# Optimization experiments

Measured on AMD Instinct MI355X. Metric: run time of the kernel, lower is better.

Reference implementation:

```python
import jax, jax.numpy as jnp
import numpy as np

B_SZ, L, D_MODEL = 2, 2048, 2048
INTER, HEADS, P, N, G, K = 4096, 64, 64, 128, 1, 4
CONV_DIM = INTER + 2 * G * N
EPS = 1e-5


def silu(x):
    return x * jax.nn.sigmoid(x)


def softplus_thresh(x, threshold=10.0):
    # matches source: where(x < thr, log(1+exp(x)), x)
    return jnp.where(x < threshold, jnp.log1p(jnp.exp(jnp.minimum(x, threshold))), x)


def setup_inputs() -> dict:
    key = jax.random.key(0)
    ks = jax.random.split(key, 8)
    s = 0.02
    return {
        "hidden_states": jax.random.normal(ks[0], (B_SZ, L, D_MODEL), jnp.float32),
        "W_z": jax.random.normal(ks[1], (D_MODEL, INTER), jnp.float32) * s,
        "W_xBC": jax.random.normal(ks[2], (D_MODEL, CONV_DIM), jnp.float32) * s,
        "W_dt": jax.random.normal(ks[3], (D_MODEL, HEADS), jnp.float32) * s,
        "conv_w": jax.random.normal(ks[4], (CONV_DIM, K), jnp.float32) * 0.1,
        "conv_b": jnp.zeros((CONV_DIM,), jnp.float32),
        "dt_bias": jax.random.uniform(ks[5], (HEADS,), jnp.float32, -2.0, 0.0),
        "A_log": jnp.log(jnp.arange(1, HEADS + 1, dtype=jnp.float32)),
        "D": jnp.ones((HEADS,), jnp.float32),
        "norm_w": jnp.ones((INTER,), jnp.float32),
        "W_out": jax.random.normal(ks[6], (INTER, D_MODEL), jnp.float32) * s,
    }


def reference(hidden_states, W_z, W_xBC, W_dt, conv_w, conv_b, dt_bias, A_log, D, norm_w, W_out):
    b, l, _ = hidden_states.shape
    Hg = HEADS // G  # heads per group

    gate = hidden_states @ W_z                      # [b,l,INTER]
    xBC = hidden_states @ W_xBC                     # [b,l,CONV_DIM]
    dt = softplus_thresh(hidden_states @ W_dt + dt_bias)  # [b,l,H]

    # causal depthwise conv1d + silu (padding=K-1, truncated to seq_len)
    xp = jnp.pad(xBC, ((0, 0), (K - 1, 0), (0, 0)))
    kern = jnp.transpose(conv_w)[:, None, :]        # [K,1,CONV_DIM] (WIO)
    xBC = jax.lax.conv_general_dilated(
        xp, kern, (1,), 'VALID',
        dimension_numbers=('NWC', 'WIO', 'NWC'),
        feature_group_count=CONV_DIM)
    xBC = silu(xBC + conv_b)

    gns = G * N
    x = xBC[..., :INTER].reshape(b, l, G, Hg, P)
    Bm = xBC[..., INTER:INTER + gns].reshape(b, l, G, N)
    Cm = xBC[..., INTER + gns:].reshape(b, l, G, N)

    A = -jnp.exp(A_log)                             # [H]
    dA = jnp.exp(dt * A).reshape(b, l, G, Hg)       # [b,l,G,Hg]
    dtx = dt.reshape(b, l, G, Hg)[..., None] * x    # [b,l,G,Hg,P]

    def step(state, inp):
        dA_t, dtx_t, B_t, C_t = inp
        # state: [b,G,Hg,P,N]
        state = state * dA_t[..., None, None] + dtx_t[..., None] * B_t[:, :, None, None, :]
        y_t = jnp.einsum('bghpn,bgn->bghp', state, C_t)
        return state, y_t

    xs = (jnp.moveaxis(dA, 1, 0), jnp.moveaxis(dtx, 1, 0),
          jnp.moveaxis(Bm, 1, 0), jnp.moveaxis(Cm, 1, 0))
    state0 = jnp.zeros((b, G, Hg, P, N), jnp.float32)
    _, ys = jax.lax.scan(step, state0, xs)          # [l,b,G,Hg,P]
    y = jnp.moveaxis(ys, 0, 1) + D.reshape(G, Hg)[..., None] * x
    scan_out = y.reshape(b, l, INTER)

    # gated RMSNorm within groups
    hs = scan_out.reshape(b, l, G, INTER // G).astype(jnp.float32)
    gt = gate.reshape(b, l, G, INTER // G).astype(jnp.float32)
    hs = hs * silu(gt)
    var = jnp.mean(hs * hs, axis=-1, keepdims=True)
    hs = hs * jax.lax.rsqrt(var + EPS)
    normed = norm_w * hs.reshape(b, l, INTER)

    return normed @ W_out
```

## Files before the change

kernel.cpp:

```cpp
#include <hip/hip_runtime.h>
#include <hip/hip_bf16.h>
#include <math.h>

typedef unsigned short u16;
typedef unsigned int   u32;
typedef __attribute__((ext_vector_type(8))) short short8;
typedef __attribute__((ext_vector_type(4))) float f32x4;

#define B_SZ     2
#define LSEQ     2048
#define DMODEL   2048
#define INTER    4096
#define HEADS    64
#define NSTATE   128
#define CONV_DIM 4352
#define XSTR     8576
#define NMAIN    8192
#define NTAILC   512
#define NTAILS   384
#define EPS      1e-5f
#define QCH      64
#define NCHUNK   (LSEQ / QCH)

__device__ __forceinline__ float bf2f(u16 u) {
    u32 v = ((u32)u) << 16;
    return __builtin_bit_cast(float, v);
}
__device__ __forceinline__ u16 f2bf(float x) {
    __hip_bfloat16 h = __float2bfloat16(x);
    return __builtin_bit_cast(u16, h);
}
__device__ __forceinline__ u32 pack2(float lo, float hi) {
    return (u32)f2bf(lo) | ((u32)f2bf(hi) << 16);
}
__device__ __forceinline__ void gl2lds16(const void* g, void* l) {
    __builtin_amdgcn_global_load_lds(
        (const __attribute__((address_space(1))) u32*)g,
        (__attribute__((address_space(3))) u32*)l, 16, 0, 0);
}

__global__ __launch_bounds__(256) void cvt_f32_bf16(
    const float* __restrict__ in, u16* __restrict__ out, int n4)
{
    int i = blockIdx.x * 256 + threadIdx.x;
    if (i >= n4) return;
    float4 v = ((const float4*)in)[i];
    ushort4 o;
    o.x = f2bf(v.x); o.y = f2bf(v.y); o.z = f2bf(v.z); o.w = f2bf(v.w);
    ((ushort4*)out)[i] = o;
}

__global__ __launch_bounds__(256) void tr_f32_bf16(
    const float* __restrict__ in, u16* __restrict__ out, int R, int C)
{
    __shared__ u16 tile[64][68];
    const int r0 = blockIdx.y * 64, c0 = blockIdx.x * 64;
    const int tr = threadIdx.x >> 4, tc = (threadIdx.x & 15) * 4;
    #pragma unroll
    for (int i = 0; i < 4; ++i) {
        int r = tr + i * 16;
        float4 v = *(const float4*)(in + (size_t)(r0 + r) * C + c0 + tc);
        tile[r][tc + 0] = f2bf(v.x);
        tile[r][tc + 1] = f2bf(v.y);
        tile[r][tc + 2] = f2bf(v.z);
        tile[r][tc + 3] = f2bf(v.w);
    }
    __syncthreads();
    #pragma unroll
    for (int i = 0; i < 4; ++i) {
        int oc = tr + i * 16;
        ushort4 o;
        o.x = tile[tc + 0][oc];
        o.y = tile[tc + 1][oc];
        o.z = tile[tc + 2][oc];
        o.w = tile[tc + 3][oc];
        *(ushort4*)(out + (size_t)(c0 + oc) * R + r0 + tc) = o;
    }
}

#define SA(c) (smem + (c) * 32768)
#define SB(c) (smem + (c) * 32768 + 16384)
#define STGA(c, q, ko) gl2lds16(gA + (size_t)((q) * 64) * lda + (ko), SA(c) + (q) * 4096 + lbase)
#define STGB(c, q, ko) gl2lds16(gB + (size_t)((q) * 64) * ldb + (ko), SB(c) + (q) * 4096 + lbase)

#define PH(mh, kk, READB, STAGES, TAIL)                                          \
  {                                                                              \
    short8 af[4];                                                                \
    _Pragma("unroll")                                                            \
    for (int i_ = 0; i_ < 4; ++i_)                                               \
      af[i_] = *(const short8*)(Ab + (wm * 128 + (mh) * 64 + i_ * 16 + lr) * 64  \
                                + ((((kk) * 4 + lq) ^ (lr & 7)) << 3));          \
    if (READB) {                                                                 \
      _Pragma("unroll")                                                          \
      for (int j_ = 0; j_ < 4; ++j_)                                             \
        bfr[kk][j_] = *(const short8*)(Bb + (wn * 64 + j_ * 16 + lr) * 64        \
                                       + ((((kk) * 4 + lq) ^ (lr & 7)) << 3));   \
    }                                                                            \
    STAGES                                                                       \
    __builtin_amdgcn_sched_barrier(0);                                           \
    __builtin_amdgcn_s_barrier();                                                \
    asm volatile("s_waitcnt lgkmcnt(0)" ::: "memory");                           \
    __builtin_amdgcn_sched_barrier(0);                                           \
    __builtin_amdgcn_s_setprio(1);                                               \
    _Pragma("unroll")                                                            \
    for (int i_ = 0; i_ < 4; ++i_)                                               \
      _Pragma("unroll")                                                          \
      for (int j_ = 0; j_ < 4; ++j_)                                             \
        acc[(mh) * 4 + i_][j_] = __builtin_amdgcn_mfma_f32_16x16x32_bf16(        \
            af[i_], bfr[kk][j_], acc[(mh) * 4 + i_][j_], 0, 0, 0);               \
    __builtin_amdgcn_s_setprio(0);                                               \
    __builtin_amdgcn_sched_barrier(0);                                           \
    TAIL                                                                         \
    __builtin_amdgcn_s_barrier();                                                \
  }

#define TILE(tt, c)                                                              \
  {                                                                              \
    const int t_ = (tt);                                                         \
    const int k1_ = (t_ + 1) << 6, k2_ = (t_ + 2) << 6;                          \
    const bool st1_ = (t_ + 1 < nt), st2_ = (t_ + 2 < nt);                       \
    const u16* Ab = SA(c); const u16* Bb = SB(c);                                \
    PH(0, 0, 1, { if (st1_) { STGA((c) ^ 1, 1, k1_); STGA((c) ^ 1, 3, k1_); } }, {}) \
    PH(1, 0, 0, { if (st1_) { STGB((c) ^ 1, 0, k1_); STGB((c) ^ 1, 1, k1_); } }, {}) \
    PH(0, 1, 1, { if (st1_) { STGB((c) ^ 1, 2, k1_); STGB((c) ^ 1, 3, k1_); } }, {}) \
    PH(1, 1, 0, { if (st2_) { STGA((c), 0, k2_); STGA((c), 2, k2_); } },         \
       { if (t_ < nt - 1) {                                                      \
           if (st2_) { asm volatile("s_waitcnt vmcnt(2)" ::: "memory"); }        \
           else      { asm volatile("s_waitcnt vmcnt(0)" ::: "memory"); } } })   \
  }

template<int OUT_BF16>
__global__ __launch_bounds__(512, 2) void gemm8(
    const u16* __restrict__ A, const u16* __restrict__ Bt, void* __restrict__ Co,
    int K, int lda, int ldb, int ldc, int Nstore)
{
    __shared__ __align__(16) u16 smem[65536];
    const int tid  = threadIdx.x;
    const int wave = tid >> 6, lane = tid & 63;
    const int wm = wave >> 2, wn = wave & 3;
    const int lr = lane & 15, lq = lane >> 4;

    const int nbx = gridDim.x;
    const int bid = blockIdx.y * nbx + blockIdx.x;
    const int nwg = nbx * gridDim.y;
    const int cpx = nwg >> 3;
    const int swz = (bid & 7) * cpx + (bid >> 3);
    const int n0 = (swz % nbx) * 256;
    const int m0 = (swz / nbx) * 256;
    const int kbase = blockIdx.z * K;

    const int srow  = tid >> 3;
    const int scb8  = ((tid & 7) ^ (srow & 7)) << 3;
    const int lbase = (tid >> 6) << 9;
    const u16* gA = A  + (size_t)(m0 + srow) * lda + kbase + scb8;
    const u16* gB = Bt + (size_t)(n0 + srow) * ldb + kbase + scb8;

    f32x4 acc[8][4];
    #pragma unroll
    for (int i = 0; i < 8; ++i)
        #pragma unroll
        for (int j = 0; j < 4; ++j) acc[i][j] = (f32x4)0.f;
    short8 bfr[2][4];

    const int nt = K >> 6;

    STGA(0, 0, 0); STGA(0, 1, 0); STGA(0, 2, 0); STGA(0, 3, 0);
    STGB(0, 0, 0); STGB(0, 1, 0); STGB(0, 2, 0); STGB(0, 3, 0);
    STGA(1, 0, 64); STGA(1, 2, 64);
    __builtin_amdgcn_sched_barrier(0);
    asm volatile("s_waitcnt vmcnt(2)" ::: "memory");
    __builtin_amdgcn_sched_barrier(0);
    __builtin_amdgcn_s_barrier();

    for (int t = 0; t < nt; t += 2) {
        TILE(t, 0)
        TILE(t + 1, 1)
    }

    const int odd = lr & 1;
    const bool wstore = (n0 + wn * 64) < Nstore;
    #pragma unroll
    for (int i = 0; i < 8; ++i)
        #pragma unroll
        for (int j = 0; j < 4; ++j) {
            float v0 = acc[i][j][0], v1 = acc[i][j][1];
            float v2 = acc[i][j][2], v3 = acc[i][j][3];
            float n0v = __shfl_xor(v0, 1), n1v = __shfl_xor(v1, 1);
            float n2v = __shfl_xor(v2, 1), n3v = __shfl_xor(v3, 1);
            int colb  = n0 + wn * 64 + j * 16 + (lr & ~1);
            int rbase = m0 + wm * 128 + i * 16 + lq * 4 + odd * 2;
            if (wstore) {
                if (OUT_BF16) {
                    u32 w0 = odd ? pack2(n2v, v2) : pack2(v0, n0v);
                    u32 w1 = odd ? pack2(n3v, v3) : pack2(v1, n1v);
                    *(u32*)((u16*)Co + (size_t)rbase * ldc + colb) = w0;
                    *(u32*)((u16*)Co + (size_t)(rbase + 1) * ldc + colb) = w1;
                } else {
                    float* Cf = (float*)Co + (size_t)blockIdx.z * 4096 * ldc;
                    float2 f0 = odd ? make_float2(n2v, v2) : make_float2(v0, n0v);
                    float2 f1 = odd ? make_float2(n3v, v3) : make_float2(v1, n1v);
                    *(float2*)(Cf + (size_t)rbase * ldc + colb) = f0;
                    *(float2*)(Cf + (size_t)(rbase + 1) * ldc + colb) = f1;
                }
            }
        }
}

__global__ __launch_bounds__(256) void tail_add(
    const float* __restrict__ Pt, u16* __restrict__ xall_)
{
    int i = blockIdx.x * 256 + threadIdx.x;
    int row = i / 96, cq = (i % 96) * 4;
    const float* p = Pt + (size_t)row * NTAILC + cq;
    const size_t zs = (size_t)4096 * NTAILC;
    float4 a = *(const float4*)(p);
    float4 b = *(const float4*)(p + zs);
    float4 c = *(const float4*)(p + 2 * zs);
    float4 d = *(const float4*)(p + 3 * zs);
    ushort4 o;
    o.x = f2bf(a.x + b.x + c.x + d.x);
    o.y = f2bf(a.y + b.y + c.y + d.y);
    o.z = f2bf(a.z + b.z + c.z + d.z);
    o.w = f2bf(a.w + b.w + c.w + d.w);
    *(ushort4*)(xall_ + (size_t)row * XSTR + NMAIN + cq) = o;
}

__global__ __launch_bounds__(256) void add2_f32(
    const float* __restrict__ a, const float* __restrict__ b,
    float* __restrict__ o, int n4)
{
    int i = blockIdx.x * 256 + threadIdx.x;
    if (i >= n4) return;
    float4 x = ((const float4*)a)[i];
    float4 y = ((const float4*)b)[i];
    x.x += y.x; x.y += y.y; x.z += y.z; x.w += y.w;
    ((float4*)o)[i] = x;
}

__global__ void dt_kernel(const u16* __restrict__ xall,
                          float* __restrict__ dtb,
                          const float* __restrict__ dt_bias, int n)
{
    int i = blockIdx.x * 256 + threadIdx.x;
    if (i >= n) return;
    int h = i & 63, row = i >> 6;
    float x = bf2f(xall[(size_t)row * XSTR + INTER + CONV_DIM + h]) + dt_bias[h];
    dtb[i] = (x < 10.f) ? log1pf(expf(x)) : x;
}

__global__ void conv_kernel(const u16* __restrict__ xall,
                            const float* __restrict__ cw,
                            const float* __restrict__ cb,
                            u16* __restrict__ xout)
{
    int c  = blockIdx.x * 256 + threadIdx.x;
    int bt = blockIdx.y;
    int t  = bt & (LSEQ - 1);
    const u16* xi = xall + (size_t)bt * XSTR + INTER + c;
    float4 w = *(const float4*)(cw + (size_t)c * 4);
    float acc = cb[c];
    acc = fmaf(bf2f(xi[0]), w.w, acc);
    if (t >= 1) acc = fmaf(bf2f(*(xi - XSTR)),     w.z, acc);
    if (t >= 2) acc = fmaf(bf2f(*(xi - 2 * XSTR)), w.y, acc);
    if (t >= 3) acc = fmaf(bf2f(*(xi - 3 * XSTR)), w.x, acc);
    xout[(size_t)bt * CONV_DIM + c] = f2bf(acc / (1.f + expf(-acc)));
}

__global__ __launch_bounds__(256) void ssd_chunk_state(
    const u16* __restrict__ xc, const float* __restrict__ dtb,
    const float* __restrict__ A_log,
    u16* __restrict__ Tg, float* __restrict__ decayQ)
{
    const int bid = blockIdx.x;
    const int b = bid >> 11, h = (bid >> 5) & 63, c = bid & 31;
    const int t0 = c * QCH;
    const int tid = threadIdx.x;
    const int wave = tid >> 6, lane = tid & 63;
    const int lr = lane & 15, lq = lane >> 4;

    __shared__ __align__(16) u16 BT[128][72];
    __shared__ __align__(16) u16 XwT[64][72];
    __shared__ float sclL[QCH];

    const u16* xg = xc + (size_t)b * LSEQ * CONV_DIM;

    if (tid < 64) {
        float dtv = dtb[((size_t)b * LSEQ + t0 + tid) * HEADS + h];
        float a = -dtv * expf(A_log[h]);
        float s = a;
        #pragma unroll
        for (int off = 1; off < 64; off <<= 1) {
            float o = __shfl_up(s, off, 64);
            if (tid >= off) s += o;
        }
        float cq = __shfl(s, 63, 64);
        sclL[tid] = dtv * expf(cq - s);
        if (tid == 0) decayQ[((b * 64 + h) << 5) + c] = expf(cq);
    }
    __syncthreads();

    #pragma unroll
    for (int r = 0; r < 16; ++r) {
        int idx = tid + 256 * r, j = idx >> 6, p = idx & 63;
        float v = bf2f(xg[(size_t)(t0 + j) * CONV_DIM + h * 64 + p]);
        XwT[p][j] = f2bf(v * sclL[j]);
    }
    #pragma unroll
    for (int r = 0; r < 32; ++r) {
        int idx = tid + 256 * r, j = idx >> 7, n = idx & 127;
        BT[n][j] = xg[(size_t)(t0 + j) * CONV_DIM + INTER + n];
    }
    __syncthreads();

    f32x4 acc[8];
    #pragma unroll
    for (int i = 0; i < 8; ++i) acc[i] = (f32x4)0.f;
    #pragma unroll
    for (int k0 = 0; k0 < QCH; k0 += 32) {
        short8 af = *(const short8*)&XwT[wave * 16 + lr][k0 + lq * 8];
        #pragma unroll
        for (int nt = 0; nt < 8; ++nt) {
            short8 bfr = *(const short8*)&BT[nt * 16 + lr][k0 + lq * 8];
            acc[nt] = __builtin_amdgcn_mfma_f32_16x16x32_bf16(af, bfr, acc[nt], 0, 0, 0);
        }
    }
    u16* To = Tg + ((((size_t)(b * 64 + h)) * NCHUNK + c) * 64) * 128;
    #pragma unroll
    for (int nt = 0; nt < 8; ++nt)
        #pragma unroll
        for (int r = 0; r < 4; ++r)
            To[(wave * 16 + lq * 4 + r) * 128 + nt * 16 + lr] = f2bf(acc[nt][r]);
}

__global__ __launch_bounds__(256) void ssd_state_scan(
    u16* __restrict__ Tg, const float* __restrict__ decayQ)
{
    const int bh = blockIdx.x >> 2, nq = blockIdx.x & 3;
    const int tid = threadIdx.x;
    const int p = tid >> 2, nb = nq * 32 + (tid & 3) * 8;
    float S[8];
    #pragma unroll
    for (int m = 0; m < 8; ++m) S[m] = 0.f;

    for (int c = 0; c < NCHUNK; ++c) {
        u16* base = Tg + ((((size_t)bh * NCHUNK + c) * 64 + p) * 128) + nb;
        uint4 tv = *(const uint4*)base;
        uint4 sv;
        sv.x = pack2(S[0], S[1]);
        sv.y = pack2(S[2], S[3]);
        sv.z = pack2(S[4], S[5]);
        sv.w = pack2(S[6], S[7]);
        *(uint4*)base = sv;
        float dq = decayQ[(bh << 5) + c];
        const u32* w = (const u32*)&tv;
        #pragma unroll
        for (int e = 0; e < 4; ++e) {
            S[e*2]     = fmaf(dq, S[e*2],     bf2f((u16)(w[e] & 0xffffu)));
            S[e*2 + 1] = fmaf(dq, S[e*2 + 1], bf2f((u16)(w[e] >> 16)));
        }
    }
}

__global__ __launch_bounds__(256) void ssd_output(
    const u16* __restrict__ xc, const float* __restrict__ dtb,
    const float* __restrict__ A_log, const float* __restrict__ Dvec,
    const u16* __restrict__ Sg,
    u16* __restrict__ y)
{
    const int bid = blockIdx.x;
    const int b = bid >> 11, h = (bid >> 5) & 63, c = bid & 31;
    const int t0 = c * QCH;
    const int tid = threadIdx.x;
    const int wave = tid >> 6, lane = tid & 63;
    const int lr = lane & 15, lq = lane >> 4;

    __shared__ __align__(16) u16 C_lds[64][136];
    __shared__ __align__(16) u16 B_lds[64][136];
    __shared__ __align__(16) u16 S_lds[64][136];
    __shared__ __align__(16) u16 P_lds[64][72];
    __shared__ __align__(16) u16 XT[64][72];
    __shared__ float cumL[QCH], dtsL[QCH], escL[QCH];

    const u16* xg = xc + (size_t)b * LSEQ * CONV_DIM;

    if (tid < 64) {
        float dtv = dtb[((size_t)b * LSEQ + t0 + tid) * HEADS + h];
        float a = -dtv * expf(A_log[h]);
        float s = a;
        #pragma unroll
        for (int off = 1; off < 64; off <<= 1) {
            float o = __shfl_up(s, off, 64);
            if (tid >= off) s += o;
        }
        cumL[tid] = s;
        dtsL[tid] = dtv;
        escL[tid] = expf(s);
    }
    #pragma unroll
    for (int r4 = 0; r4 < 4; ++r4) {
        int idx4 = tid + 256 * r4;
        int j = idx4 >> 4, c8 = (idx4 & 15) * 8;
        *(uint4*)&B_lds[j][c8] = *(const uint4*)(xg + (size_t)(t0 + j) * CONV_DIM + INTER + c8);
        *(uint4*)&C_lds[j][c8] = *(const uint4*)(xg + (size_t)(t0 + j) * CONV_DIM + INTER + NSTATE + c8);
        *(uint4*)&S_lds[j][c8] = *(const uint4*)(Sg + ((((size_t)(b * 64 + h)) * NCHUNK + c) * 64 + j) * 128 + c8);
    }
    #pragma unroll
    for (int r = 0; r < 16; ++r) {
        int idx = tid + 256 * r, j = idx >> 6, p = idx & 63;
        XT[p][j] = xg[(size_t)(t0 + j) * CONV_DIM + h * 64 + p];
    }
    __syncthreads();

    f32x4 accG[4];
    #pragma unroll
    for (int i = 0; i < 4; ++i) accG[i] = (f32x4)0.f;
    #pragma unroll
    for (int k0 = 0; k0 < NSTATE; k0 += 32) {
        short8 af = *(const short8*)&C_lds[wave * 16 + lr][k0 + lq * 8];
        #pragma unroll
        for (int jt = 0; jt < 4; ++jt) {
            short8 bfr = *(const short8*)&B_lds[jt * 16 + lr][k0 + lq * 8];
            accG[jt] = __builtin_amdgcn_mfma_f32_16x16x32_bf16(af, bfr, accG[jt], 0, 0, 0);
        }
    }
    #pragma unroll
    for (int jt = 0; jt < 4; ++jt)
        #pragma unroll
        for (int r = 0; r < 4; ++r) {
            int ii = wave * 16 + lq * 4 + r;
            int jj = jt * 16 + lr;
            float v = (jj <= ii)
                ? accG[jt][r] * dtsL[jj] * expf(cumL[ii] - cumL[jj]) : 0.f;
            P_lds[ii][jj] = f2bf(v);
        }
    __syncthreads();

    f32x4 accY[4], accZ[4];
    #pragma unroll
    for (int i = 0; i < 4; ++i) { accY[i] = (f32x4)0.f; accZ[i] = (f32x4)0.f; }
    #pragma unroll
    for (int k0 = 0; k0 < QCH; k0 += 32) {
        short8 af = *(const short8*)&P_lds[wave * 16 + lr][k0 + lq * 8];
        #pragma unroll
        for (int pt = 0; pt < 4; ++pt) {
            short8 bfr = *(const short8*)&XT[pt * 16 + lr][k0 + lq * 8];
            accY[pt] = __builtin_amdgcn_mfma_f32_16x16x32_bf16(af, bfr, accY[pt], 0, 0, 0);
        }
    }
    #pragma unroll
    for (int k0 = 0; k0 < NSTATE; k0 += 32) {
        short8 af = *(const short8*)&C_lds[wave * 16 + lr][k0 + lq * 8];
        #pragma unroll
        for (int pt = 0; pt < 4; ++pt) {
            short8 bfr = *(const short8*)&S_lds[pt * 16 + lr][k0 + lq * 8];
            accZ[pt] = __builtin_amdgcn_mfma_f32_16x16x32_bf16(af, bfr, accZ[pt], 0, 0, 0);
        }
    }

    const float Dh = Dvec[h];
    u16* yg = y + ((size_t)b * LSEQ + t0) * XSTR + h * 64;
    #pragma unroll
    for (int pt = 0; pt < 4; ++pt)
        #pragma unroll
        for (int r = 0; r < 4; ++r) {
            int ii = wave * 16 + lq * 4 + r;
            int pp = pt * 16 + lr;
            float xv = bf2f(XT[pp][ii]);
            float o = accY[pt][r] + escL[ii] * accZ[pt][r] + Dh * xv;
            yg[(size_t)ii * XSTR + pp] = f2bf(o);
        }
}

__global__ __launch_bounds__(256) void norm_kernel(
    u16* __restrict__ xall, const float* __restrict__ w)
{
    const int row = blockIdx.x;
    const u16* yr = xall + (size_t)row * XSTR + INTER;
    u16*       gr = xall + (size_t)row * XSTR;
    const int tid = threadIdx.x;

    float v[16];
    float ss = 0.f;
    #pragma unroll
    for (int i = 0; i < 16; ++i) {
        int idx = tid + i * 256;
        float hv = bf2f(yr[idx]);
        float g  = bf2f(gr[idx]);
        float val = hv * (g / (1.f + expf(-g)));
        v[i] = val;
        ss = fmaf(val, val, ss);
    }
    #pragma unroll
    for (int o = 32; o > 0; o >>= 1) ss += __shfl_xor(ss, o);
    __shared__ float part[4];
    if ((tid & 63) == 0) part[tid >> 6] = ss;
    __syncthreads();
    float tot  = part[0] + part[1] + part[2] + part[3];
    float rinv = rsqrtf(tot * (1.f / INTER) + EPS);
    #pragma unroll
    for (int i = 0; i < 16; ++i) {
        int idx = tid + i * 256;
        gr[idx] = f2bf(w[idx] * v[i] * rinv);
    }
}

extern "C" void kernel_launch(void* const* d_in, const int* in_sizes, int n_in,
                              void* d_out, int out_size, void* d_ws, size_t ws_size,
                              hipStream_t stream)
{
    const float* hs      = (const float*)d_in[0];
    const float* W_z     = (const float*)d_in[1];
    const float* W_xBC   = (const float*)d_in[2];
    const float* W_dt    = (const float*)d_in[3];
    const float* conv_w  = (const float*)d_in[4];
    const float* conv_b  = (const float*)d_in[5];
    const float* dt_bias = (const float*)d_in[6];
    const float* A_log   = (const float*)d_in[7];
    const float* Dv      = (const float*)d_in[8];
    const float* norm_w  = (const float*)d_in[9];
    const float* W_out   = (const float*)d_in[10];
    float* out = (float*)d_out;
    char*  w8  = (char*)d_ws;

    u16* hs_bf  = (u16*)(w8 + 0);
    u16* Wt_all = (u16*)(w8 + 16777216);
    u16* Tbuf   = (u16*)(w8 + 0);
    float* Cpart= (float*)(w8 + 0);
    u16* Wt_out = (u16*)(w8 + 67108864);
    u16* xall   = (u16*)(w8 + 83886080);
    u16* xconv  = (u16*)(w8 + 154140672);
    float* Ptail= (float*)(w8 + 154140672);
    float* dtb  = (float*)(w8 + 189792256);
    float* dcq  = (float*)(w8 + 190840832);

    const int M = B_SZ * LSEQ;

    cvt_f32_bf16<<<(M * DMODEL / 4 + 255) / 256, 256, 0, stream>>>(hs, hs_bf, M * DMODEL / 4);
    tr_f32_bf16<<<dim3(INTER / 64,    DMODEL / 64), 256, 0, stream>>>(W_z,   Wt_all, DMODEL, INTER);
    tr_f32_bf16<<<dim3(CONV_DIM / 64, DMODEL / 64), 256, 0, stream>>>(W_xBC, Wt_all + (size_t)INTER * DMODEL, DMODEL, CONV_DIM);
    tr_f32_bf16<<<dim3(1,             DMODEL / 64), 256, 0, stream>>>(W_dt,  Wt_all + (size_t)(INTER + CONV_DIM) * DMODEL, DMODEL, 64);
    hipMemsetAsync(Wt_all + (size_t)(INTER + CONV_DIM + 64) * DMODEL, 0, (size_t)192 * DMODEL * 2, stream);
    tr_f32_bf16<<<dim3(DMODEL / 64,   INTER / 64),  256, 0, stream>>>(W_out, Wt_out, INTER, DMODEL);

    gemm8<1><<<dim3(NMAIN / 256, M / 256, 1), 512, 0, stream>>>(
        hs_bf, Wt_all, (void*)xall, DMODEL , DMODEL, DMODEL,
        XSTR , NMAIN );
    gemm8<0><<<dim3(NTAILC / 256, M / 256, 4), 512, 0, stream>>>(
        hs_bf, Wt_all + (size_t)NMAIN * DMODEL, (void*)Ptail, DMODEL / 4 ,
        DMODEL, DMODEL, NTAILC , NTAILS );
    tail_add<<<M * (NTAILS / 4) / 256, 256, 0, stream>>>(Ptail, xall);

    dt_kernel<<<(M * HEADS + 255) / 256, 256, 0, stream>>>(xall, dtb, dt_bias, M * HEADS);
    conv_kernel<<<dim3(CONV_DIM / 256, M), 256, 0, stream>>>(xall, conv_w, conv_b, xconv);

    ssd_chunk_state<<<B_SZ * HEADS * NCHUNK, 256, 0, stream>>>(xconv, dtb, A_log, Tbuf, dcq);
    ssd_state_scan<<<B_SZ * HEADS * 4, 256, 0, stream>>>(Tbuf, dcq);
    ssd_output<<<B_SZ * HEADS * NCHUNK, 256, 0, stream>>>(xconv, dtb, A_log, Dv, Tbuf, xall + INTER);

    norm_kernel<<<M, 256, 0, stream>>>(xall, norm_w);

    gemm8<0><<<dim3(DMODEL / 256, M / 256, 2), 512, 0, stream>>>(
        xall, Wt_out, (void*)Cpart, INTER / 2 , XSTR ,
        INTER , DMODEL , DMODEL );
    add2_f32<<<(M * DMODEL / 4 + 255) / 256, 256, 0, stream>>>(
        Cpart, Cpart + (size_t)M * DMODEL, out, M * DMODEL / 4);
}
```

Before: 610.5 us.

## Simplify GEMM pipeline to plain double buffering, vectorize conv and norm kernels

Replaces the hand-interleaved four-phase GEMM main loop, which staggered global-to-LDS stages between MFMA phases, with a simple double-buffered loop: issue all next-tile loads, compute the current tile, then wait for everything and barrier. It also vectorizes the depthwise conv kernel to four channels per thread and the gated RMSNorm kernel to 8-element loads and stores. The GEMM change gives up fine-grained overlap of loads with MFMA and barrier placement in exchange for simpler code, while the two elementwise kernels are meant to cut memory transaction count.

Result: slower. 624.0 us (+2.2%).

```diff
diff --git a/kernel.cpp b/kernel.cpp
--- a/kernel.cpp
+++ b/kernel.cpp
@@ -83,52 +83,6 @@
 #define STGA(c, q, ko) gl2lds16(gA + (size_t)((q) * 64) * lda + (ko), SA(c) + (q) * 4096 + lbase)
 #define STGB(c, q, ko) gl2lds16(gB + (size_t)((q) * 64) * ldb + (ko), SB(c) + (q) * 4096 + lbase)
 
-#define PH(mh, kk, READB, STAGES, TAIL)                                          \
-  {                                                                              \
-    short8 af[4];                                                                \
-    _Pragma("unroll")                                                            \
-    for (int i_ = 0; i_ < 4; ++i_)                                               \
-      af[i_] = *(const short8*)(Ab + (wm * 128 + (mh) * 64 + i_ * 16 + lr) * 64  \
-                                + ((((kk) * 4 + lq) ^ (lr & 7)) << 3));          \
-    if (READB) {                                                                 \
-      _Pragma("unroll")                                                          \
-      for (int j_ = 0; j_ < 4; ++j_)                                             \
-        bfr[kk][j_] = *(const short8*)(Bb + (wn * 64 + j_ * 16 + lr) * 64        \
-                                       + ((((kk) * 4 + lq) ^ (lr & 7)) << 3));   \
-    }                                                                            \
-    STAGES                                                                       \
-    __builtin_amdgcn_sched_barrier(0);                                           \
-    __builtin_amdgcn_s_barrier();                                                \
-    asm volatile("s_waitcnt lgkmcnt(0)" ::: "memory");                           \
-    __builtin_amdgcn_sched_barrier(0);                                           \
-    __builtin_amdgcn_s_setprio(1);                                               \
-    _Pragma("unroll")                                                            \
-    for (int i_ = 0; i_ < 4; ++i_)                                               \
-      _Pragma("unroll")                                                          \
-      for (int j_ = 0; j_ < 4; ++j_)                                             \
-        acc[(mh) * 4 + i_][j_] = __builtin_amdgcn_mfma_f32_16x16x32_bf16(        \
-            af[i_], bfr[kk][j_], acc[(mh) * 4 + i_][j_], 0, 0, 0);               \
-    __builtin_amdgcn_s_setprio(0);                                               \
-    __builtin_amdgcn_sched_barrier(0);                                           \
-    TAIL                                                                         \
-    __builtin_amdgcn_s_barrier();                                                \
-  }
-
-#define TILE(tt, c)                                                              \
-  {                                                                              \
-    const int t_ = (tt);                                                         \
-    const int k1_ = (t_ + 1) << 6, k2_ = (t_ + 2) << 6;                          \
-    const bool st1_ = (t_ + 1 < nt), st2_ = (t_ + 2 < nt);                       \
-    const u16* Ab = SA(c); const u16* Bb = SB(c);                                \
-    PH(0, 0, 1, { if (st1_) { STGA((c) ^ 1, 1, k1_); STGA((c) ^ 1, 3, k1_); } }, {}) \
-    PH(1, 0, 0, { if (st1_) { STGB((c) ^ 1, 0, k1_); STGB((c) ^ 1, 1, k1_); } }, {}) \
-    PH(0, 1, 1, { if (st1_) { STGB((c) ^ 1, 2, k1_); STGB((c) ^ 1, 3, k1_); } }, {}) \
-    PH(1, 1, 0, { if (st2_) { STGA((c), 0, k2_); STGA((c), 2, k2_); } },         \
-       { if (t_ < nt - 1) {                                                      \
-           if (st2_) { asm volatile("s_waitcnt vmcnt(2)" ::: "memory"); }        \
-           else      { asm volatile("s_waitcnt vmcnt(0)" ::: "memory"); } } })   \
-  }
-
 template<int OUT_BF16>
 __global__ __launch_bounds__(512, 2) void gemm8(
     const u16* __restrict__ A, const u16* __restrict__ Bt, void* __restrict__ Co,
@@ -160,21 +114,51 @@
     for (int i = 0; i < 8; ++i)
         #pragma unroll
         for (int j = 0; j < 4; ++j) acc[i][j] = (f32x4)0.f;
-    short8 bfr[2][4];
 
     const int nt = K >> 6;
 
     STGA(0, 0, 0); STGA(0, 1, 0); STGA(0, 2, 0); STGA(0, 3, 0);
     STGB(0, 0, 0); STGB(0, 1, 0); STGB(0, 2, 0); STGB(0, 3, 0);
-    STGA(1, 0, 64); STGA(1, 2, 64);
     __builtin_amdgcn_sched_barrier(0);
-    asm volatile("s_waitcnt vmcnt(2)" ::: "memory");
-    __builtin_amdgcn_sched_barrier(0);
+    asm volatile("s_waitcnt vmcnt(0)" ::: "memory");
     __builtin_amdgcn_s_barrier();
 
-    for (int t = 0; t < nt; t += 2) {
-        TILE(t, 0)
-        TILE(t + 1, 1)
+    for (int t = 0; t < nt; ++t) {
+        const int c = t & 1;
+        if (t + 1 < nt) {
+            const int k1 = (t + 1) << 6;
+            STGA(c ^ 1, 0, k1); STGA(c ^ 1, 1, k1);
+            STGA(c ^ 1, 2, k1); STGA(c ^ 1, 3, k1);
+            STGB(c ^ 1, 0, k1); STGB(c ^ 1, 1, k1);
+            STGB(c ^ 1, 2, k1); STGB(c ^ 1, 3, k1);
+        }
+        __builtin_amdgcn_sched_barrier(0);
+        const u16* Ab = SA(c);
+        const u16* Bb = SB(c);
+        #pragma unroll
+        for (int kk = 0; kk < 2; ++kk) {
+            short8 a8[8], b4[4];
+            #pragma unroll
+            for (int i = 0; i < 8; ++i)
+                a8[i] = *(const short8*)(Ab + (wm * 128 + i * 16 + lr) * 64
+                                         + ((((kk) * 4 + lq) ^ (lr & 7)) << 3));
+            #pragma unroll
+            for (int j = 0; j < 4; ++j)
+                b4[j] = *(const short8*)(Bb + (wn * 64 + j * 16 + lr) * 64
+                                         + ((((kk) * 4 + lq) ^ (lr & 7)) << 3));
+            __builtin_amdgcn_s_setprio(1);
+            #pragma unroll
+            for (int i = 0; i < 8; ++i)
+                #pragma unroll
+                for (int j = 0; j < 4; ++j)
+                    acc[i][j] = __builtin_amdgcn_mfma_f32_16x16x32_bf16(
+                        a8[i], b4[j], acc[i][j], 0, 0, 0);
+            __builtin_amdgcn_s_setprio(0);
+        }
+        if (t + 1 < nt) {
+            asm volatile("s_waitcnt vmcnt(0)" ::: "memory");
+            __builtin_amdgcn_s_barrier();
+        }
     }
 
     const int odd = lr & 1;
@@ -248,22 +232,46 @@
     dtb[i] = (x < 10.f) ? log1pf(expf(x)) : x;
 }
 
-__global__ void conv_kernel(const u16* __restrict__ xall,
-                            const float* __restrict__ cw,
-                            const float* __restrict__ cb,
-                            u16* __restrict__ xout)
-{
-    int c  = blockIdx.x * 256 + threadIdx.x;
+__global__ __launch_bounds__(256) void conv_kernel(
+    const u16* __restrict__ xall, const float* __restrict__ cw,
+    const float* __restrict__ cb, u16* __restrict__ xout)
+{
+    int c4 = blockIdx.x * 256 + threadIdx.x;
+    if (c4 >= CONV_DIM / 4) return;
+    int c  = c4 * 4;
     int bt = blockIdx.y;
     int t  = bt & (LSEQ - 1);
     const u16* xi = xall + (size_t)bt * XSTR + INTER + c;
-    float4 w = *(const float4*)(cw + (size_t)c * 4);
-    float acc = cb[c];
-    acc = fmaf(bf2f(xi[0]), w.w, acc);
-    if (t >= 1) acc = fmaf(bf2f(*(xi - XSTR)),     w.z, acc);
-    if (t >= 2) acc = fmaf(bf2f(*(xi - 2 * XSTR)), w.y, acc);
-    if (t >= 3) acc = fmaf(bf2f(*(xi - 3 * XSTR)), w.x, acc);
-    xout[(size_t)bt * CONV_DIM + c] = f2bf(acc / (1.f + expf(-acc)));
+    float4 w0 = *(const float4*)(cw + (size_t)(c + 0) * 4);
+    float4 w1 = *(const float4*)(cw + (size_t)(c + 1) * 4);
+    float4 w2 = *(const float4*)(cw + (size_t)(c + 2) * 4);
+    float4 w3 = *(const float4*)(cw + (size_t)(c + 3) * 4);
+    float4 bb = *(const float4*)(cb + c);
+    float a0 = bb.x, a1 = bb.y, a2 = bb.z, a3 = bb.w;
+    ushort4 x0 = *(const ushort4*)(xi);
+    a0 = fmaf(bf2f(x0.x), w0.w, a0); a1 = fmaf(bf2f(x0.y), w1.w, a1);
+    a2 = fmaf(bf2f(x0.z), w2.w, a2); a3 = fmaf(bf2f(x0.w), w3.w, a3);
+    if (t >= 1) {
+        ushort4 xm = *(const ushort4*)(xi - XSTR);
+        a0 = fmaf(bf2f(xm.x), w0.z, a0); a1 = fmaf(bf2f(xm.y), w1.z, a1);
+        a2 = fmaf(bf2f(xm.z), w2.z, a2); a3 = fmaf(bf2f(xm.w), w3.z, a3);
+    }
+    if (t >= 2) {
+        ushort4 xm = *(const ushort4*)(xi - 2 * XSTR);
+        a0 = fmaf(bf2f(xm.x), w0.y, a0); a1 = fmaf(bf2f(xm.y), w1.y, a1);
+        a2 = fmaf(bf2f(xm.z), w2.y, a2); a3 = fmaf(bf2f(xm.w), w3.y, a3);
+    }
+    if (t >= 3) {
+        ushort4 xm = *(const ushort4*)(xi - 3 * XSTR);
+        a0 = fmaf(bf2f(xm.x), w0.x, a0); a1 = fmaf(bf2f(xm.y), w1.x, a1);
+        a2 = fmaf(bf2f(xm.z), w2.x, a2); a3 = fmaf(bf2f(xm.w), w3.x, a3);
+    }
+    ushort4 o;
+    o.x = f2bf(a0 / (1.f + expf(-a0)));
+    o.y = f2bf(a1 / (1.f + expf(-a1)));
+    o.z = f2bf(a2 / (1.f + expf(-a2)));
+    o.w = f2bf(a3 / (1.f + expf(-a3)));
+    *(ushort4*)(xout + (size_t)bt * CONV_DIM + c) = o;
 }
 
 __global__ __launch_bounds__(256) void ssd_chunk_state(
@@ -482,13 +490,20 @@
     float v[16];
     float ss = 0.f;
     #pragma unroll
-    for (int i = 0; i < 16; ++i) {
-        int idx = tid + i * 256;
-        float hv = bf2f(yr[idx]);
-        float g  = bf2f(gr[idx]);
-        float val = hv * (g / (1.f + expf(-g)));
-        v[i] = val;
-        ss = fmaf(val, val, ss);
+    for (int i = 0; i < 2; ++i) {
+        int e0 = i * 2048 + tid * 8;
+        uint4 hv4 = *(const uint4*)(yr + e0);
+        uint4 gv4 = *(const uint4*)(gr + e0);
+        const u16* hp = (const u16*)&hv4;
+        const u16* gp = (const u16*)&gv4;
+        #pragma unroll
+        for (int k = 0; k < 8; ++k) {
+            float hv = bf2f(hp[k]);
+            float g  = bf2f(gp[k]);
+            float val = hv * (g / (1.f + expf(-g)));
+            v[i * 8 + k] = val;
+            ss = fmaf(val, val, ss);
+        }
     }
     #pragma unroll
     for (int o = 32; o > 0; o >>= 1) ss += __shfl_xor(ss, o);
@@ -498,9 +513,16 @@
     float tot  = part[0] + part[1] + part[2] + part[3];
     float rinv = rsqrtf(tot * (1.f / INTER) + EPS);
     #pragma unroll
-    for (int i = 0; i < 16; ++i) {
-        int idx = tid + i * 256;
-        gr[idx] = f2bf(w[idx] * v[i] * rinv);
+    for (int i = 0; i < 2; ++i) {
+        int e0 = i * 2048 + tid * 8;
+        float4 wa = *(const float4*)(w + e0);
+        float4 wb = *(const float4*)(w + e0 + 4);
+        uint4 sv;
+        sv.x = pack2(wa.x * v[i*8+0] * rinv, wa.y * v[i*8+1] * rinv);
+        sv.y = pack2(wa.z * v[i*8+2] * rinv, wa.w * v[i*8+3] * rinv);
+        sv.z = pack2(wb.x * v[i*8+4] * rinv, wb.y * v[i*8+5] * rinv);
+        sv.w = pack2(wb.z * v[i*8+6] * rinv, wb.w * v[i*8+7] * rinv);
+        *(uint4*)(gr + e0) = sv;
     }
 }
 
@@ -551,7 +573,7 @@
     tail_add<<<M * (NTAILS / 4) / 256, 256, 0, stream>>>(Ptail, xall);
 
     dt_kernel<<<(M * HEADS + 255) / 256, 256, 0, stream>>>(xall, dtb, dt_bias, M * HEADS);
-    conv_kernel<<<dim3(CONV_DIM / 256, M), 256, 0, stream>>>(xall, conv_w, conv_b, xconv);
+    conv_kernel<<<dim3((CONV_DIM / 4 + 255) / 256, M), 256, 0, stream>>>(xall, conv_w, conv_b, xconv);
 
     ssd_chunk_state<<<B_SZ * HEADS * NCHUNK, 256, 0, stream>>>(xconv, dtb, A_log, Tbuf, dcq);
     ssd_state_scan<<<B_SZ * HEADS * 4, 256, 0, stream>>>(Tbuf, dcq);
```
